# Performance work log

Hardware: AMD Instinct MI355X
Metric: run time of the kernel (lower is better)

Reference implementation:

```python
import jax, jax.numpy as jnp
import numpy as np

B, T, N = 16, 256, 20000
REGIONS, TOPK = 20000, 0.2
IN_DIM = int(REGIONS * TOPK ** 2)   # 800
K = int(REGIONS * TOPK)             # 4000
R = 1000                            # rest_limitation
ZCOLS = K + R                       # all-False mask columns per sample


def setup_inputs() -> dict:
    key = jax.random.key(0)
    ks = jax.random.split(key, 8)
    x = jax.random.normal(ks[0], (B, T, IN_DIM), jnp.float32)
    # first ZCOLS voxel columns are never covered (mask False), rest are covered
    border_mask = jnp.concatenate(
        [jnp.zeros((B, T, ZCOLS), bool), jnp.ones((B, T, N - ZCOLS), bool)], axis=-1)
    # K distinct indices per sample, drawn from the uncovered columns [0, ZCOLS)
    index = jax.vmap(lambda k: jax.random.permutation(k, ZCOLS)[:K])(
        jax.random.split(ks[1], B)).astype(jnp.int32)
    s1 = 1.0 / np.sqrt(IN_DIM); s2 = 1.0 / np.sqrt(K)
    W1 = jax.random.uniform(ks[2], (IN_DIM, K), jnp.float32, -s1, s1)
    b1 = jax.random.uniform(ks[3], (K,), jnp.float32, -s1, s1)
    W2 = jax.random.uniform(ks[4], (K, K), jnp.float32, -s2, s2)
    b2 = jax.random.uniform(ks[5], (K,), jnp.float32, -s2, s2)
    W3 = jax.random.uniform(ks[6], (K, R), jnp.float32, -s2, s2)
    b3 = jax.random.uniform(ks[7], (R,), jnp.float32, -s2, s2)
    return dict(x=x, border_mask=border_mask, index=index,
                W1=W1, b1=b1, W2=W2, b2=b2, W3=W3, b3=b3)


def reference(x, border_mask, index, W1, b1, W2, b2, W3, b3):
    h = x @ W1 + b1                  # unzip   [B,T,K]
    h = h @ W2 + b2                  # unprocess [B,T,K]
    x_rest = h @ W3 + b3             # rest    [B,T,R]
    colsum = border_mask.sum(axis=1)                 # [B,N] per-voxel coverage count
    idx_member = jax.vmap(lambda i: jnp.zeros((N,), bool).at[i].set(True))(index)
    # scatter h into indexed voxel columns
    x_recon = jax.vmap(lambda i, hb: jnp.zeros((T, N), h.dtype).at[:, i].set(hb))(index, h)
    # rest positions: uncovered columns not already taken by index (sorted order)
    rest_mask = (colsum == 0) & ~idx_member          # [B,N]
    rank = jnp.cumsum(rest_mask, axis=-1) - 1        # position among rest columns
    valid = rest_mask & (rank < R)                   # cap at rest_limitation ('adjust')
    g = jnp.take_along_axis(
        x_rest, jnp.broadcast_to(jnp.clip(rank, 0, R - 1)[:, None, :], (B, T, N)), axis=-1)
    return jnp.where(valid[:, None, :], g, x_recon)
```

## Files before the change

kernel.cpp:

```cpp
#include <hip/hip_runtime.h>

typedef __attribute__((ext_vector_type(4))) float f32x4;
typedef __attribute__((ext_vector_type(8))) __bf16 bf16x8;

#define B_SZ   16
#define T_SZ   256
#define BT_SZ  4096
#define N_VOX  20000
#define INDIM  800
#define K1P    896
#define K_DIM  4000
#define KP     4096
#define R_DIM  1000
#define RP     1024
#define SPLITK 4

__device__ __forceinline__ unsigned short f2bf(float f) {
  unsigned int u = __builtin_bit_cast(unsigned int, f);
  u += 0x7fffu + ((u >> 16) & 1u);
  return (unsigned short)(u >> 16);
}
__device__ __forceinline__ float bf2f(unsigned short h) {
  unsigned int u = ((unsigned int)h) << 16;
  return __builtin_bit_cast(float, u);
}
__device__ __forceinline__ void gload16(const void* g, void* l) {
  __builtin_amdgcn_global_load_lds(
      (const __attribute__((address_space(1))) void*)g,
      (__attribute__((address_space(3))) void*)l, 16, 0, 0);
}

__global__ void cvt_pad_x(const float* __restrict__ src,
                          unsigned short* __restrict__ dst) {
  int row = blockIdx.x;
  int c4 = threadIdx.x;
  if (c4 >= K1P / 4) return;
  ushort4 o = {0, 0, 0, 0};
  if (c4 < INDIM / 4) {
    float4 v = ((const float4*)(src + (size_t)row * INDIM))[c4];
    o.x = f2bf(v.x); o.y = f2bf(v.y); o.z = f2bf(v.z); o.w = f2bf(v.w);
  }
  ((ushort4*)(dst + (size_t)row * K1P))[c4] = o;
}

__global__ void transpose_cvt(const float* __restrict__ W,
                              unsigned short* __restrict__ WT,
                              int K, int N, int Kpad, int Npad) {
  __shared__ float tile[32][33];
  int k0 = blockIdx.x * 32, n0 = blockIdx.y * 32;
  for (int i = threadIdx.y; i < 32; i += 8) {
    int k = k0 + i, n = n0 + threadIdx.x;
    tile[i][threadIdx.x] = (k < K && n < N) ? W[(size_t)k * N + n] : 0.f;
  }
  __syncthreads();
  for (int i = threadIdx.y; i < 32; i += 8) {
    int n = n0 + i, k = k0 + threadIdx.x;
    if (n < Npad && k < Kpad)
      WT[(size_t)n * Kpad + k] = f2bf(tile[threadIdx.x][i]);
  }
}

__global__ void covered_kernel(const int* __restrict__ bmask,
                               unsigned char* __restrict__ cov) {
  int n4 = blockIdx.x * 256 + threadIdx.x;
  int b = blockIdx.y;
  if (n4 >= N_VOX / 4) return;
  const int4* p = (const int4*)(bmask + (size_t)b * T_SZ * N_VOX) + n4;
  int4 a = {0, 0, 0, 0};
  for (int t0 = 0; t0 < T_SZ; t0 += 8) {
    int4 c[8];
#pragma unroll
    for (int tt = 0; tt < 8; ++tt)
      c[tt] = p[(size_t)(t0 + tt) * (N_VOX / 4)];
#pragma unroll
    for (int tt = 0; tt < 8; ++tt) {
      a.x |= c[tt].x; a.y |= c[tt].y; a.z |= c[tt].z; a.w |= c[tt].w;
    }
    if (a.x && a.y && a.z && a.w) break;
  }
  uchar4 o;
  o.x = (unsigned char)(a.x != 0); o.y = (unsigned char)(a.y != 0);
  o.z = (unsigned char)(a.z != 0); o.w = (unsigned char)(a.w != 0);
  *(uchar4*)(cov + (size_t)b * N_VOX + (size_t)n4 * 4) = o;
}

__global__ void map_kernel(const int* __restrict__ index,
                           const unsigned char* __restrict__ cov,
                           int* __restrict__ srcmap) {
  int b = blockIdx.x, tid = threadIdx.x;
  int* sm = srcmap + (size_t)b * N_VOX;
  for (int n = tid; n < N_VOX; n += 1024) sm[n] = -1;
  __syncthreads();
  const int* idx = index + (size_t)b * K_DIM;
  for (int j = tid; j < K_DIM; j += 1024) sm[idx[j]] = j;
  __syncthreads();

  __shared__ int wsum[16];
  __shared__ int s_running;
  if (tid == 0) s_running = 0;
  __syncthreads();
  const int lane = tid & 63, wid = tid >> 6;
  const unsigned char* cv = cov + (size_t)b * N_VOX;
  for (int base = 0; base < N_VOX; base += 1024) {
    int n = base + tid;
    bool flag = (n < N_VOX) && (!cv[n]) && (sm[n] < 0);
    unsigned long long bal = __ballot(flag);
    if (lane == 0) wsum[wid] = __popcll(bal);
    __syncthreads();
    int woff = 0, tot = 0;
    for (int w = 0; w < 16; ++w) {
      int c = wsum[w];
      if (w < wid) woff += c;
      tot += c;
    }
    int rank = s_running + woff + __popcll(bal & ((1ull << lane) - 1ull));
    if (flag && rank < R_DIM) sm[n] = K_DIM + rank;
    __syncthreads();
    if (tid == 0) s_running += tot;
    __syncthreads();
  }
}

template <int BM, bool SPLIT>
__global__ __launch_bounds__(256) void gemm_bt(
    const unsigned short* __restrict__ A,
    const unsigned short* __restrict__ BTm,
    const float* __restrict__ bias, int nbias,
    unsigned short* __restrict__ C,
    int K, int lda, int ldb, int ldc, size_t zstride) {
  constexpr int MI = BM / 32;
  __shared__ __align__(16) unsigned short As[BM * 32];
  __shared__ __align__(16) unsigned short Bs[128 * 32];
  const int tid = threadIdx.x;
  const int wid = tid >> 6;
  const int lane = tid & 63;
  const int bm = blockIdx.y, bn = blockIdx.x;
  if (SPLIT) {
    int kz = blockIdx.z;
    A += (size_t)kz * K;
    BTm += (size_t)kz * K;
    C += (size_t)kz * zstride;
  }
  const int wm = wid >> 1, wn = wid & 1;
  const int sub = lane >> 2;
  const int quad = lane & 3;

  const int rA0 = wid * 16 + sub;
  const char* gA0 = (const char*)(A + (size_t)(bm * BM + rA0) * lda) + quad * 16;
  const char* gA1 = (const char*)(A + (size_t)(bm * BM + ((BM == 128) ? rA0 + 64 : rA0)) * lda) + quad * 16;
  const char* gB0 = (const char*)(BTm + (size_t)(bn * 128 + rA0) * ldb) + quad * 16;
  const char* gB1 = (const char*)(BTm + (size_t)(bn * 128 + rA0 + 64) * ldb) + quad * 16;

  char* lA0 = (char*)As + wid * 1024 + lane * 16;
  char* lA1 = lA0 + 4096;
  char* lB0 = (char*)Bs + wid * 1024 + lane * 16;
  char* lB1 = lB0 + 4096;

  const int r15 = lane & 15;
  const int kg = lane >> 4;

  f32x4 acc[MI][4] = {};

  for (int kt = 0; kt < K; kt += 32) {
    const int kb = kt * 2;
    gload16(gA0 + kb, lA0);
    if constexpr (BM == 128) gload16(gA1 + kb, lA1);
    gload16(gB0 + kb, lB0);
    gload16(gB1 + kb, lB1);
    __syncthreads();
    bf16x8 af[MI], bfr[4];
#pragma unroll
    for (int i = 0; i < MI; ++i)
      af[i] = *(const bf16x8*)&As[(wm * (BM / 2) + i * 16 + r15) * 32 + kg * 8];
#pragma unroll
    for (int j = 0; j < 4; ++j)
      bfr[j] = *(const bf16x8*)&Bs[(wn * 64 + j * 16 + r15) * 32 + kg * 8];
#pragma unroll
    for (int i = 0; i < MI; ++i)
#pragma unroll
      for (int j = 0; j < 4; ++j)
        acc[i][j] = __builtin_amdgcn_mfma_f32_16x16x32_bf16(af[i], bfr[j], acc[i][j], 0, 0, 0);
    __syncthreads();
  }

#pragma unroll
  for (int i = 0; i < MI; ++i) {
    const int row0 = bm * BM + wm * (BM / 2) + i * 16 + kg * 4;
#pragma unroll
    for (int j = 0; j < 4; ++j) {
      const int col = bn * 128 + wn * 64 + j * 16 + r15;
      float bv = 0.f;
      if constexpr (!SPLIT) bv = bias[(col < nbias) ? col : (nbias - 1)];
#pragma unroll
      for (int r = 0; r < 4; ++r)
        C[(size_t)(row0 + r) * ldc + col] = f2bf(acc[i][j][r] + bv);
    }
  }
}

__global__ void reduce_splitk(const unsigned short* __restrict__ part,
                              const float* __restrict__ bias,
                              unsigned short* __restrict__ out) {
  int i = blockIdx.x * 256 + threadIdx.x;
  if (i >= BT_SZ * RP / 4) return;
  const size_t zs = (size_t)BT_SZ * RP / 4;
  float s[4] = {0.f, 0.f, 0.f, 0.f};
#pragma unroll
  for (int z = 0; z < SPLITK; ++z) {
    ushort4 p = ((const ushort4*)part)[z * zs + i];
    s[0] += bf2f(p.x); s[1] += bf2f(p.y); s[2] += bf2f(p.z); s[3] += bf2f(p.w);
  }
  int col = (i * 4) & (RP - 1);
  ushort4 o;
  o.x = f2bf(s[0] + bias[(col     < R_DIM) ? col     : R_DIM - 1]);
  o.y = f2bf(s[1] + bias[(col + 1 < R_DIM) ? col + 1 : R_DIM - 1]);
  o.z = f2bf(s[2] + bias[(col + 2 < R_DIM) ? col + 2 : R_DIM - 1]);
  o.w = f2bf(s[3] + bias[(col + 3 < R_DIM) ? col + 3 : R_DIM - 1]);
  ((ushort4*)out)[i] = o;
}

__global__ __launch_bounds__(512, 2) void gemm256(
    const unsigned short* __restrict__ A,
    const unsigned short* __restrict__ BTm,
    const float* __restrict__ bias, int nbias,
    unsigned short* __restrict__ C,
    int K, int lda, int ldb, int ldc) {
  __shared__ __align__(16) char smem[131072];
  const int tid = threadIdx.x;
  const int wid = tid >> 6, lane = tid & 63;
  const int wm = wid >> 2, wn = wid & 3;
  const int r15 = lane & 15, kg = lane >> 4;
  const int bm = blockIdx.y, bn = blockIdx.x;

  const int srow = tid >> 2;
  const int scol = ((tid & 3) * 8) ^ ((srow & 8) ? 16 : 0);
  const unsigned short* gA = A + (size_t)(bm * 256 + srow) * lda + scol;
  const unsigned short* gB = BTm + (size_t)(bn * 256 + srow) * ldb + scol;

  const int cxor = (kg * 16) ^ ((r15 & 8) ? 32 : 0);
  const int aoff = (wm * 128 + r15) * 64 + cxor;
  const int boff = (wn * 64 + r15) * 64 + cxor;

  f32x4 acc[8][4] = {};
  bf16x8 bfr[4];

#define STAGE_HALF(S, MAT, KH, TN)                                            \
  {                                                                           \
    const unsigned short* g =                                                 \
        ((MAT) ? gB : gA) + (size_t)(TN) * 64 + (KH) * 32;                    \
    char* l = smem + (S) * 65536 + (MAT) * 32768 + (KH) * 16384 + tid * 16;   \
    gload16(g, l);                                                            \
    gload16(g + (size_t)128 * ((MAT) ? ldb : lda), l + 8192);                 \
  }

#define PHASE(S, KS, MH, TN, DOVM)                                            \
  {                                                                           \
    bf16x8 af[4];                                                             \
    if ((MH) == 0) {                                                          \
      _Pragma("unroll")                                                       \
      for (int j = 0; j < 4; ++j)                                             \
        bfr[j] = *(const bf16x8*)(smem + (S) * 65536 + 32768 +                \
                                  (KS) * 16384 + boff + j * 1024);            \
    }                                                                         \
    _Pragma("unroll")                                                         \
    for (int i = 0; i < 4; ++i)                                               \
      af[i] = *(const bf16x8*)(smem + (S) * 65536 + (KS) * 16384 +            \
                               (MH) * 4096 + aoff + i * 1024);                \
    STAGE_HALF((S) ^ 1, (MH), (KS), TN)                                       \
    if (DOVM) asm volatile("s_waitcnt vmcnt(4)" ::: "memory");                \
    asm volatile("s_barrier" ::: "memory");                                   \
    __builtin_amdgcn_s_setprio(1);                                            \
    _Pragma("unroll")                                                         \
    for (int i = 0; i < 4; ++i)                                               \
      _Pragma("unroll")                                                       \
      for (int j = 0; j < 4; ++j)                                             \
        acc[(MH) * 4 + i][j] = __builtin_amdgcn_mfma_f32_16x16x32_bf16(       \
            af[i], bfr[j], acc[(MH) * 4 + i][j], 0, 0, 0);                    \
    __builtin_amdgcn_s_setprio(0);                                            \
    asm volatile("s_barrier" ::: "memory");                                   \
  }

#define TILE4(S, TN)                                                          \
  PHASE(S, 0, 0, TN, 0)                                                       \
  PHASE(S, 0, 1, TN, 1)                                                       \
  PHASE(S, 1, 0, TN, 0)                                                       \
  PHASE(S, 1, 1, TN, 1)

  const int NT = K >> 6;
  STAGE_HALF(0, 0, 0, 0)
  STAGE_HALF(0, 1, 0, 0)
  STAGE_HALF(0, 0, 1, 0)
  STAGE_HALF(0, 1, 1, 0)
  asm volatile("s_waitcnt vmcnt(4)" ::: "memory");
  asm volatile("s_barrier" ::: "memory");

  for (int tp = 0; tp < NT; tp += 2) {
    const int tn1 = tp + 1;
    TILE4(0, tn1)
    const int tn2 = (tp + 2 < NT) ? tp + 2 : NT - 1;
    TILE4(1, tn2)
  }

#undef STAGE_HALF
#undef PHASE
#undef TILE4

#pragma unroll
  for (int f = 0; f < 8; ++f) {
    const int row0 = bm * 256 + wm * 128 + f * 16 + kg * 4;
#pragma unroll
    for (int j = 0; j < 4; ++j) {
      const int col = bn * 256 + wn * 64 + j * 16 + r15;
      const float bv = bias[(col < nbias) ? col : (nbias - 1)];
#pragma unroll
      for (int r = 0; r < 4; ++r)
        C[(size_t)(row0 + r) * ldc + col] = f2bf(acc[f][j][r] + bv);
    }
  }
}

__global__ void fill_out(const int* __restrict__ srcmap,
                         const unsigned short* __restrict__ h2b,
                         const unsigned short* __restrict__ xrb,
                         float* __restrict__ out) {
  int n4 = blockIdx.x * 256 + threadIdx.x;
  if (n4 >= N_VOX / 4) return;
  int t = blockIdx.y, b = blockIdx.z;
  size_t bt = (size_t)b * T_SZ + t;
  const int4 sm = ((const int4*)(srcmap + (size_t)b * N_VOX))[n4];
  const unsigned short* hrow = h2b + bt * KP;
  const unsigned short* xrow = xrb + bt * RP;
  f32x4 v;
  v.x = (sm.x < 0) ? 0.f : bf2f(sm.x < K_DIM ? hrow[sm.x] : xrow[sm.x - K_DIM]);
  v.y = (sm.y < 0) ? 0.f : bf2f(sm.y < K_DIM ? hrow[sm.y] : xrow[sm.y - K_DIM]);
  v.z = (sm.z < 0) ? 0.f : bf2f(sm.z < K_DIM ? hrow[sm.z] : xrow[sm.z - K_DIM]);
  v.w = (sm.w < 0) ? 0.f : bf2f(sm.w < K_DIM ? hrow[sm.w] : xrow[sm.w - K_DIM]);
  __builtin_nontemporal_store(v, (f32x4*)(out + bt * N_VOX) + n4);
}

extern "C" void kernel_launch(void* const* d_in, const int* in_sizes, int n_in,
                              void* d_out, int out_size, void* d_ws, size_t ws_size,
                              hipStream_t stream) {
  const float* x          = (const float*)d_in[0];
  const int* bm           = (const int*)d_in[1];
  const int* index        = (const int*)d_in[2];
  const float* W1         = (const float*)d_in[3];
  const float* b1         = (const float*)d_in[4];
  const float* W2         = (const float*)d_in[5];
  const float* b2         = (const float*)d_in[6];
  const float* W3         = (const float*)d_in[7];
  const float* b3         = (const float*)d_in[8];
  float* out = (float*)d_out;

  char* ws = (char*)d_ws;
  size_t off = 0;
  auto alloc = [&](size_t bytes) -> void* {
    void* p = ws + off;
    off += (bytes + 255) & ~(size_t)255;
    return p;
  };
  unsigned short* xb   = (unsigned short*)alloc((size_t)BT_SZ * K1P * 2);
  unsigned short* w1t  = (unsigned short*)alloc((size_t)KP * K1P * 2);
  unsigned short* w2t  = (unsigned short*)alloc((size_t)KP * KP * 2);
  unsigned short* w3t  = (unsigned short*)alloc((size_t)RP * KP * 2);
  unsigned short* h1b  = (unsigned short*)alloc((size_t)BT_SZ * KP * 2);
  unsigned short* h2b  = (unsigned short*)alloc((size_t)BT_SZ * KP * 2);
  unsigned short* xrb  = (unsigned short*)alloc((size_t)BT_SZ * RP * 2);
  unsigned short* xpart = (unsigned short*)alloc((size_t)SPLITK * BT_SZ * RP * 2);
  unsigned char* cov = (unsigned char*)alloc((size_t)B_SZ * N_VOX);
  int* srcmap = (int*)alloc((size_t)B_SZ * N_VOX * 4);

  cvt_pad_x<<<BT_SZ, 256, 0, stream>>>(x, xb);
  {
    dim3 g(K1P / 32, KP / 32);
    transpose_cvt<<<g, dim3(32, 8), 0, stream>>>(W1, w1t, INDIM, K_DIM, K1P, KP);
  }
  {
    dim3 g(KP / 32, KP / 32);
    transpose_cvt<<<g, dim3(32, 8), 0, stream>>>(W2, w2t, K_DIM, K_DIM, KP, KP);
  }
  {
    dim3 g(KP / 32, RP / 32);
    transpose_cvt<<<g, dim3(32, 8), 0, stream>>>(W3, w3t, K_DIM, R_DIM, KP, RP);
  }

  {
    dim3 g((N_VOX / 4 + 255) / 256, B_SZ);
    covered_kernel<<<g, 256, 0, stream>>>(bm, cov);
  }
  map_kernel<<<B_SZ, 1024, 0, stream>>>(index, cov, srcmap);

  {
    dim3 g(KP / 256, BT_SZ / 256);
    gemm256<<<g, 512, 0, stream>>>(xb, w1t, b1, K_DIM, h1b, K1P, K1P, K1P, KP);
  }
  {
    dim3 g(KP / 256, BT_SZ / 256);
    gemm256<<<g, 512, 0, stream>>>(h1b, w2t, b2, K_DIM, h2b, KP, KP, KP, KP);
  }
  {
    dim3 g(RP / 128, BT_SZ / 128, SPLITK);
    gemm_bt<128, true><<<g, 256, 0, stream>>>(h2b, w3t, nullptr, 0, xpart,
                                              KP / SPLITK, KP, KP, RP,
                                              (size_t)BT_SZ * RP);
  }
  reduce_splitk<<<(BT_SZ * RP / 4 + 255) / 256, 256, 0, stream>>>(xpart, b3, xrb);

  {
    dim3 g((N_VOX / 4 + 255) / 256, T_SZ, B_SZ);
    fill_out<<<g, 256, 0, stream>>>(srcmap, h2b, xrb, out);
  }
}
```

Measured before the change: 433.1 us.

## Merge prep kernels into one launch and fold split-K reduction into fill_out

```diff
diff --git a/kernel.cpp b/kernel.cpp
--- a/kernel.cpp
+++ b/kernel.cpp
@@ -30,58 +30,91 @@
       (__attribute__((address_space(3))) void*)l, 16, 0, 0);
 }
 
-__global__ void cvt_pad_x(const float* __restrict__ src,
-                          unsigned short* __restrict__ dst) {
-  int row = blockIdx.x;
-  int c4 = threadIdx.x;
-  if (c4 >= K1P / 4) return;
-  ushort4 o = {0, 0, 0, 0};
-  if (c4 < INDIM / 4) {
-    float4 v = ((const float4*)(src + (size_t)row * INDIM))[c4];
-    o.x = f2bf(v.x); o.y = f2bf(v.y); o.z = f2bf(v.z); o.w = f2bf(v.w);
-  }
-  ((ushort4*)(dst + (size_t)row * K1P))[c4] = o;
-}
-
-__global__ void transpose_cvt(const float* __restrict__ W,
+#define PREP_CVT    4096
+#define PREP_W1     3584
+#define PREP_W2     16384
+#define PREP_W3     4096
+#define PREP_COV    320
+
+__device__ void dev_transpose(const float* __restrict__ W,
                               unsigned short* __restrict__ WT,
-                              int K, int N, int Kpad, int Npad) {
+                              int K, int N, int Kpad, int Npad,
+                              int kb, int nb, int tx, int ty,
+                              float (*tile)[33]) {
+  int k0 = kb * 32, n0 = nb * 32;
+  for (int i = ty; i < 32; i += 8) {
+    int k = k0 + i, n = n0 + tx;
+    tile[i][tx] = (k < K && n < N) ? W[(size_t)k * N + n] : 0.f;
+  }
+  __syncthreads();
+  for (int i = ty; i < 32; i += 8) {
+    int n = n0 + i, k = k0 + tx;
+    if (n < Npad && k < Kpad)
+      WT[(size_t)n * Kpad + k] = f2bf(tile[tx][i]);
+  }
+}
+
+__global__ __launch_bounds__(256) void prep_kernel(
+    const float* __restrict__ x, unsigned short* __restrict__ xb,
+    const float* __restrict__ W1, unsigned short* __restrict__ w1t,
+    const float* __restrict__ W2, unsigned short* __restrict__ w2t,
+    const float* __restrict__ W3, unsigned short* __restrict__ w3t,
+    const int* __restrict__ bmask, unsigned char* __restrict__ cov) {
   __shared__ float tile[32][33];
-  int k0 = blockIdx.x * 32, n0 = blockIdx.y * 32;
-  for (int i = threadIdx.y; i < 32; i += 8) {
-    int k = k0 + i, n = n0 + threadIdx.x;
-    tile[i][threadIdx.x] = (k < K && n < N) ? W[(size_t)k * N + n] : 0.f;
-  }
-  __syncthreads();
-  for (int i = threadIdx.y; i < 32; i += 8) {
-    int n = n0 + i, k = k0 + threadIdx.x;
-    if (n < Npad && k < Kpad)
-      WT[(size_t)n * Kpad + k] = f2bf(tile[threadIdx.x][i]);
-  }
-}
-
-__global__ void covered_kernel(const int* __restrict__ bmask,
-                               unsigned char* __restrict__ cov) {
-  int n4 = blockIdx.x * 256 + threadIdx.x;
-  int b = blockIdx.y;
-  if (n4 >= N_VOX / 4) return;
-  const int4* p = (const int4*)(bmask + (size_t)b * T_SZ * N_VOX) + n4;
-  int4 a = {0, 0, 0, 0};
-  for (int t0 = 0; t0 < T_SZ; t0 += 8) {
-    int4 c[8];
-#pragma unroll
-    for (int tt = 0; tt < 8; ++tt)
-      c[tt] = p[(size_t)(t0 + tt) * (N_VOX / 4)];
-#pragma unroll
-    for (int tt = 0; tt < 8; ++tt) {
-      a.x |= c[tt].x; a.y |= c[tt].y; a.z |= c[tt].z; a.w |= c[tt].w;
+  int id = blockIdx.x;
+  const int tid = threadIdx.x;
+  const int tx = tid & 31, ty = tid >> 5;
+
+  if (id < PREP_CVT) {
+    int row = id, c4 = tid;
+    if (c4 < K1P / 4) {
+      ushort4 o = {0, 0, 0, 0};
+      if (c4 < INDIM / 4) {
+        float4 v = ((const float4*)(x + (size_t)row * INDIM))[c4];
+        o.x = f2bf(v.x); o.y = f2bf(v.y); o.z = f2bf(v.z); o.w = f2bf(v.w);
+      }
+      ((ushort4*)(xb + (size_t)row * K1P))[c4] = o;
     }
-    if (a.x && a.y && a.z && a.w) break;
-  }
-  uchar4 o;
-  o.x = (unsigned char)(a.x != 0); o.y = (unsigned char)(a.y != 0);
-  o.z = (unsigned char)(a.z != 0); o.w = (unsigned char)(a.w != 0);
-  *(uchar4*)(cov + (size_t)b * N_VOX + (size_t)n4 * 4) = o;
+    return;
+  }
+  id -= PREP_CVT;
+  if (id < PREP_W1) {
+    dev_transpose(W1, w1t, INDIM, K_DIM, K1P, KP, id % 28, id / 28, tx, ty, tile);
+    return;
+  }
+  id -= PREP_W1;
+  if (id < PREP_W2) {
+    dev_transpose(W2, w2t, K_DIM, K_DIM, KP, KP, id % 128, id / 128, tx, ty, tile);
+    return;
+  }
+  id -= PREP_W2;
+  if (id < PREP_W3) {
+    dev_transpose(W3, w3t, K_DIM, R_DIM, KP, RP, id % 128, id / 128, tx, ty, tile);
+    return;
+  }
+  id -= PREP_W3;
+  {
+    int n4 = (id % 20) * 256 + tid;
+    int b = id / 20;
+    if (n4 >= N_VOX / 4) return;
+    const int4* p = (const int4*)(bmask + (size_t)b * T_SZ * N_VOX) + n4;
+    int4 a = {0, 0, 0, 0};
+    for (int t0 = 0; t0 < T_SZ; t0 += 8) {
+      int4 c[8];
+#pragma unroll
+      for (int tt = 0; tt < 8; ++tt)
+        c[tt] = p[(size_t)(t0 + tt) * (N_VOX / 4)];
+#pragma unroll
+      for (int tt = 0; tt < 8; ++tt) {
+        a.x |= c[tt].x; a.y |= c[tt].y; a.z |= c[tt].z; a.w |= c[tt].w;
+      }
+      if (a.x && a.y && a.z && a.w) break;
+    }
+    uchar4 o;
+    o.x = (unsigned char)(a.x != 0); o.y = (unsigned char)(a.y != 0);
+    o.z = (unsigned char)(a.z != 0); o.w = (unsigned char)(a.w != 0);
+    *(uchar4*)(cov + (size_t)b * N_VOX + (size_t)n4 * 4) = o;
+  }
 }
 
 __global__ void map_kernel(const int* __restrict__ index,
@@ -196,27 +229,6 @@
         C[(size_t)(row0 + r) * ldc + col] = f2bf(acc[i][j][r] + bv);
     }
   }
-}
-
-__global__ void reduce_splitk(const unsigned short* __restrict__ part,
-                              const float* __restrict__ bias,
-                              unsigned short* __restrict__ out) {
-  int i = blockIdx.x * 256 + threadIdx.x;
-  if (i >= BT_SZ * RP / 4) return;
-  const size_t zs = (size_t)BT_SZ * RP / 4;
-  float s[4] = {0.f, 0.f, 0.f, 0.f};
-#pragma unroll
-  for (int z = 0; z < SPLITK; ++z) {
-    ushort4 p = ((const ushort4*)part)[z * zs + i];
-    s[0] += bf2f(p.x); s[1] += bf2f(p.y); s[2] += bf2f(p.z); s[3] += bf2f(p.w);
-  }
-  int col = (i * 4) & (RP - 1);
-  ushort4 o;
-  o.x = f2bf(s[0] + bias[(col     < R_DIM) ? col     : R_DIM - 1]);
-  o.y = f2bf(s[1] + bias[(col + 1 < R_DIM) ? col + 1 : R_DIM - 1]);
-  o.z = f2bf(s[2] + bias[(col + 2 < R_DIM) ? col + 2 : R_DIM - 1]);
-  o.w = f2bf(s[3] + bias[(col + 3 < R_DIM) ? col + 3 : R_DIM - 1]);
-  ((ushort4*)out)[i] = o;
 }
 
 __global__ __launch_bounds__(512, 2) void gemm256(
@@ -321,7 +333,8 @@
 
 __global__ void fill_out(const int* __restrict__ srcmap,
                          const unsigned short* __restrict__ h2b,
-                         const unsigned short* __restrict__ xrb,
+                         const unsigned short* __restrict__ xpart,
+                         const float* __restrict__ b3,
                          float* __restrict__ out) {
   int n4 = blockIdx.x * 256 + threadIdx.x;
   if (n4 >= N_VOX / 4) return;
@@ -329,12 +342,19 @@
   size_t bt = (size_t)b * T_SZ + t;
   const int4 sm = ((const int4*)(srcmap + (size_t)b * N_VOX))[n4];
   const unsigned short* hrow = h2b + bt * KP;
-  const unsigned short* xrow = xrb + bt * RP;
+  const unsigned short* xrow = xpart + bt * RP;
+  const size_t zs = (size_t)BT_SZ * RP;
+  auto val = [&](int s) -> float {
+    if (s < 0) return 0.f;
+    if (s < K_DIM) return bf2f(hrow[s]);
+    int r = s - K_DIM;
+    float acc = b3[r];
+#pragma unroll
+    for (int z = 0; z < SPLITK; ++z) acc += bf2f(xrow[z * zs + r]);
+    return acc;
+  };
   f32x4 v;
-  v.x = (sm.x < 0) ? 0.f : bf2f(sm.x < K_DIM ? hrow[sm.x] : xrow[sm.x - K_DIM]);
-  v.y = (sm.y < 0) ? 0.f : bf2f(sm.y < K_DIM ? hrow[sm.y] : xrow[sm.y - K_DIM]);
-  v.z = (sm.z < 0) ? 0.f : bf2f(sm.z < K_DIM ? hrow[sm.z] : xrow[sm.z - K_DIM]);
-  v.w = (sm.w < 0) ? 0.f : bf2f(sm.w < K_DIM ? hrow[sm.w] : xrow[sm.w - K_DIM]);
+  v.x = val(sm.x); v.y = val(sm.y); v.z = val(sm.z); v.w = val(sm.w);
   __builtin_nontemporal_store(v, (f32x4*)(out + bt * N_VOX) + n4);
 }
 
@@ -359,34 +379,19 @@
     off += (bytes + 255) & ~(size_t)255;
     return p;
   };
-  unsigned short* xb   = (unsigned short*)alloc((size_t)BT_SZ * K1P * 2);
-  unsigned short* w1t  = (unsigned short*)alloc((size_t)KP * K1P * 2);
-  unsigned short* w2t  = (unsigned short*)alloc((size_t)KP * KP * 2);
-  unsigned short* w3t  = (unsigned short*)alloc((size_t)RP * KP * 2);
-  unsigned short* h1b  = (unsigned short*)alloc((size_t)BT_SZ * KP * 2);
-  unsigned short* h2b  = (unsigned short*)alloc((size_t)BT_SZ * KP * 2);
-  unsigned short* xrb  = (unsigned short*)alloc((size_t)BT_SZ * RP * 2);
+  unsigned short* xb    = (unsigned short*)alloc((size_t)BT_SZ * K1P * 2);
+  unsigned short* w1t   = (unsigned short*)alloc((size_t)KP * K1P * 2);
+  unsigned short* w2t   = (unsigned short*)alloc((size_t)KP * KP * 2);
+  unsigned short* w3t   = (unsigned short*)alloc((size_t)RP * KP * 2);
+  unsigned short* h1b   = (unsigned short*)alloc((size_t)BT_SZ * KP * 2);
+  unsigned short* h2b   = (unsigned short*)alloc((size_t)BT_SZ * KP * 2);
   unsigned short* xpart = (unsigned short*)alloc((size_t)SPLITK * BT_SZ * RP * 2);
   unsigned char* cov = (unsigned char*)alloc((size_t)B_SZ * N_VOX);
   int* srcmap = (int*)alloc((size_t)B_SZ * N_VOX * 4);
 
-  cvt_pad_x<<<BT_SZ, 256, 0, stream>>>(x, xb);
-  {
-    dim3 g(K1P / 32, KP / 32);
-    transpose_cvt<<<g, dim3(32, 8), 0, stream>>>(W1, w1t, INDIM, K_DIM, K1P, KP);
-  }
-  {
-    dim3 g(KP / 32, KP / 32);
-    transpose_cvt<<<g, dim3(32, 8), 0, stream>>>(W2, w2t, K_DIM, K_DIM, KP, KP);
-  }
-  {
-    dim3 g(KP / 32, RP / 32);
-    transpose_cvt<<<g, dim3(32, 8), 0, stream>>>(W3, w3t, K_DIM, R_DIM, KP, RP);
-  }
-
-  {
-    dim3 g((N_VOX / 4 + 255) / 256, B_SZ);
-    covered_kernel<<<g, 256, 0, stream>>>(bm, cov);
+  {
+    int nblk = PREP_CVT + PREP_W1 + PREP_W2 + PREP_W3 + PREP_COV;
+    prep_kernel<<<nblk, 256, 0, stream>>>(x, xb, W1, w1t, W2, w2t, W3, w3t, bm, cov);
   }
   map_kernel<<<B_SZ, 1024, 0, stream>>>(index, cov, srcmap);
 
@@ -404,10 +409,9 @@
                                               KP / SPLITK, KP, KP, RP,
                                               (size_t)BT_SZ * RP);
   }
-  reduce_splitk<<<(BT_SZ * RP / 4 + 255) / 256, 256, 0, stream>>>(xpart, b3, xrb);
 
   {
     dim3 g((N_VOX / 4 + 255) / 256, T_SZ, B_SZ);
-    fill_out<<<g, 256, 0, stream>>>(srcmap, h2b, xrb, out);
-  }
-}
+    fill_out<<<g, 256, 0, stream>>>(srcmap, h2b, xpart, b3, out);
+  }
+}
```

Measured after the change: 433.6 us. Within noise of the previous version (+0.1%).
